# Kernel optimization log

Hardware: AMD Instinct MI355X
Metric: run time of the kernel (lower is better)

## Reference

```python
import jax, jax.numpy as jnp
import numpy as np

B, D, HW, Z, PATCH = 16, 768, 32, 256, 16
N = HW * HW          # input_token_num = 1024
TOPK = N // 2        # topk=0.5 -> 512
EPS = 1e-5

def setup_inputs() -> dict:
    key = jax.random.key(0)
    ks = jax.random.split(key, 9)
    s = 0.02
    return {
        'image_features': jax.random.normal(ks[0], (B, D, HW, HW), jnp.float32),
        'w1': jax.random.normal(ks[1], (D, D), jnp.float32) * s,
        'b1': jnp.zeros((D,), jnp.float32),
        'w2': jax.random.normal(ks[2], (D, 1), jnp.float32) * s,
        'b2': jnp.zeros((1,), jnp.float32),
        'wp': jax.random.normal(ks[3], (D, Z), jnp.float32) * s,   # pre_projection
        'bp': jnp.zeros((Z,), jnp.float32),
        'mask_token': jnp.zeros((Z, 1), jnp.float32),              # init mode 0
        'conv_w': jax.random.normal(ks[4], (Z, Z), jnp.float32) * s,  # post_projection 1x1
        'conv_b': jnp.zeros((Z,), jnp.float32),
    }

def _upsample_nearest(m, f):
    # (B,1,h,w) -> (B,1,h*f,w*f)
    return jnp.repeat(jnp.repeat(m, f, axis=2), f, axis=3)

def reference(image_features, w1, b1, w2, b2, wp, bp, mask_token, conv_w, conv_b):
    x = image_features.transpose(0, 2, 3, 1).reshape(B, N, D)  # B (H W) C
    # score MLP: Linear-ReLU-Linear-Sigmoid
    h = jax.nn.relu(jnp.einsum('bnd,de->bne', x, w1) + b1)
    pred_score = jax.nn.sigmoid(jnp.einsum('bnd,de->bne', h, w2) + b2).reshape(B, N)
    score_sg = jax.lax.stop_gradient(pred_score)  # clone().detach()
    order = jnp.argsort(-score_sg, axis=1)        # descending sort
    top = order[:, :TOPK]                          # (B, K) int
    # LayerNorm (no affine) over channel dim
    mu = x.mean(-1, keepdims=True)
    var = x.var(-1, keepdims=True)
    xn = (x - mu) * jax.lax.rsqrt(var + EPS)
    # gather topk tokens, weight by (non-detached) score
    gathered = jnp.take_along_axis(xn, top[..., None], axis=1)
    gathered = gathered * jnp.take_along_axis(pred_score, top, axis=1)[..., None]
    sample_h = (jnp.einsum('bkd,dz->bkz', gathered, wp) + bp).transpose(0, 2, 1)  # B Z K
    # binary mask: scatter ones at topk positions
    mask = jnp.zeros((B, N), jnp.float32).at[jnp.arange(B)[:, None], top].set(1.0)
    binary_map = _upsample_nearest(mask.reshape(B, 1, HW, HW), PATCH)
    # normalized score map (global min/max over whole batch)
    smin, smax = score_sg.min(), score_sg.max()
    normed = (score_sg - smin) / jnp.maximum(smax - smin, EPS)
    score_map = _upsample_nearest(normed.reshape(B, 1, HW, HW), PATCH)
    # postforward: fill all N slots with mask_token, scatter sample_h at topk slots
    base = jnp.broadcast_to(mask_token, (Z, N))
    emb = jax.vmap(lambda hi, idx: base.at[:, idx].set(hi))(sample_h, top)  # (B,Z,N)
    emb = emb.reshape(B, Z, HW, HW)
    dec = jnp.einsum('oz,bzhw->bohw', conv_w, emb) + conv_b[None, :, None, None]
    return dec, binary_map, score_map
```

## Files before the change

### kernel.cpp

```cpp
#include <hip/hip_runtime.h>
#include <hip/hip_bf16.h>
#include <math.h>

#define B_ 16
#define D_ 768
#define N_ 1024
#define Z_ 256
#define TOPK_ 512
#define HW_ 32
#define EPS_ 1e-5f

typedef unsigned int uint;
typedef unsigned short ushort;
typedef __attribute__((ext_vector_type(4))) short short4v;
typedef __attribute__((ext_vector_type(8))) short bf16x8;
typedef __attribute__((ext_vector_type(4))) float f32x4;
typedef __attribute__((ext_vector_type(4))) int int4v;

__device__ __forceinline__ ushort f2bf(float v) {
  uint b = __float_as_uint(v);
  b += 0x7FFFu + ((b >> 16) & 1u);
  return (ushort)(b >> 16);
}
__device__ __forceinline__ float bf2f(ushort h) { return __uint_as_float(((uint)h) << 16); }
__device__ __forceinline__ int pk2(ushort a, ushort b) { return (int)((uint)a | ((uint)b << 16)); }

__global__ __launch_bounds__(256) void k_pre1(const float* __restrict__ conv_w,
                                              const float* __restrict__ conv_b,
                                              const float* __restrict__ bp,
                                              const float* __restrict__ mtk,
                                              float* __restrict__ db,
                                              float* __restrict__ bg) {
  int o = threadIdx.x;
  float a1 = 0.f, a2 = 0.f;
  for (int z = 0; z < Z_; ++z) {
    float c = conv_w[o * Z_ + z];
    a1 += c * bp[z];
    a2 += c * mtk[z];
  }
  db[o] = conv_b[o] + a1;
  bg[o] = conv_b[o] + a2;
}

__global__ __launch_bounds__(64) void k_w1pack(const float* __restrict__ w1,
                                               short* __restrict__ wA) {
  int lane = threadIdx.x;
  int f = blockIdx.x;
  int eg = f / 24, kkg = f % 24;
  int e = eg * 16 + (lane & 15);
  int d0 = kkg * 32 + 8 * (lane >> 4);
  ushort hh[8], ll[8];
#pragma unroll
  for (int j = 0; j < 8; ++j) {
    float v = w1[(size_t)(d0 + j) * D_ + e];
    hh[j] = f2bf(v);
    ll[j] = f2bf(v - bf2f(hh[j]));
  }
  int4v ph = {pk2(hh[0],hh[1]), pk2(hh[2],hh[3]), pk2(hh[4],hh[5]), pk2(hh[6],hh[7])};
  int4v pl = {pk2(ll[0],ll[1]), pk2(ll[2],ll[3]), pk2(ll[4],ll[5]), pk2(ll[6],ll[7])};
  int4v* W = (int4v*)wA;
  W[(size_t)f * 128 + lane] = ph;
  W[(size_t)f * 128 + 64 + lane] = pl;
}

__global__ __launch_bounds__(64) void k_mtpack(const float* __restrict__ wp,
                                               const float* __restrict__ conv_w,
                                               short* __restrict__ mtA) {
  int lane = threadIdx.x;
  int f = blockIdx.x;
  int og = f / 24, kkg = f % 24;
  int o = og * 16 + (lane & 15);
  int d0 = kkg * 32 + 8 * (lane >> 4);
  float acc[8] = {0.f,0.f,0.f,0.f,0.f,0.f,0.f,0.f};
  for (int z = 0; z < Z_; ++z) {
    float c = conv_w[o * Z_ + z];
#pragma unroll
    for (int j = 0; j < 8; ++j) acc[j] += wp[(size_t)(d0 + j) * Z_ + z] * c;
  }
  int4v p = {pk2(f2bf(acc[0]),f2bf(acc[1])), pk2(f2bf(acc[2]),f2bf(acc[3])),
             pk2(f2bf(acc[4]),f2bf(acc[5])), pk2(f2bf(acc[6]),f2bf(acc[7]))};
  ((int4v*)mtA)[(size_t)f * 64 + lane] = p;
}

__global__ __launch_bounds__(512, 2) void k_score_mfma(const float* __restrict__ xin,
                                                       const short* __restrict__ wA,
                                                       const float* __restrict__ b1,
                                                       const float* __restrict__ w2,
                                                       const float* __restrict__ b2,
                                                       float* __restrict__ score) {
  __shared__ short panH[64 * 128];
  __shared__ short panL[64 * 128];
  __shared__ float red[8][4][16];
  int tid = threadIdx.x;
  int wave = tid >> 6, lane = tid & 63;
  int g = lane >> 4, cc = lane & 15;
  int b = blockIdx.x >> 4;
  int n0 = (blockIdx.x & 15) * 64;
  const float* xb = xin + (size_t)b * D_ * N_ + n0;
  int qt = tid & 15, qd = tid >> 4;
  int t0 = qt * 4, dl0 = qd * 4;
  f32x4 acc[6][4];
#pragma unroll
  for (int et = 0; et < 6; ++et)
#pragma unroll
    for (int tn = 0; tn < 4; ++tn) acc[et][tn] = (f32x4){0.f,0.f,0.f,0.f};
  const int4v* Ab = (const int4v*)wA;
  for (int kc = 0; kc < 6; ++kc) {
    float4 v0 = *(const float4*)(xb + (size_t)(kc*128 + dl0 + 0) * N_ + t0);
    float4 v1 = *(const float4*)(xb + (size_t)(kc*128 + dl0 + 1) * N_ + t0);
    float4 v2 = *(const float4*)(xb + (size_t)(kc*128 + dl0 + 2) * N_ + t0);
    float4 v3 = *(const float4*)(xb + (size_t)(kc*128 + dl0 + 3) * N_ + t0);
    __syncthreads();
#define STG(j, e0, e1, e2, e3) { \
    int t = t0 + (j); \
    int sb = t * 128 + (dl0 ^ ((t & 7) << 3)); \
    ushort h0 = f2bf(e0), h1 = f2bf(e1), h2 = f2bf(e2), h3 = f2bf(e3); \
    short4v ph = {(short)h0,(short)h1,(short)h2,(short)h3}; \
    short4v pl = {(short)f2bf((e0)-bf2f(h0)), (short)f2bf((e1)-bf2f(h1)), \
                  (short)f2bf((e2)-bf2f(h2)), (short)f2bf((e3)-bf2f(h3))}; \
    *(short4v*)&panH[sb] = ph; \
    *(short4v*)&panL[sb] = pl; }
    STG(0, v0.x, v1.x, v2.x, v3.x)
    STG(1, v0.y, v1.y, v2.y, v3.y)
    STG(2, v0.z, v1.z, v2.z, v3.z)
    STG(3, v0.w, v1.w, v2.w, v3.w)
#undef STG
    __syncthreads();
#pragma unroll
    for (int kk = 0; kk < 4; ++kk) {
      bf16x8 Bh[4], Bl[4];
#pragma unroll
      for (int tn = 0; tn < 4; ++tn) {
        int t = tn * 16 + cc;
        int sb = t * 128 + ((kk * 32 + 8 * g) ^ ((t & 7) << 3));
        Bh[tn] = *(const bf16x8*)&panH[sb];
        Bl[tn] = *(const bf16x8*)&panL[sb];
      }
#pragma unroll
      for (int et = 0; et < 6; ++et) {
        size_t fidx = ((size_t)((wave * 6 + et) * 24 + (kc * 4 + kk))) * 128 + lane;
        union { int4v i; bf16x8 v; } ah, al;
        ah.i = Ab[fidx];
        al.i = Ab[fidx + 64];
#pragma unroll
        for (int tn = 0; tn < 4; ++tn) {
          acc[et][tn] = __builtin_amdgcn_mfma_f32_16x16x32_bf16(ah.v, Bh[tn], acc[et][tn], 0, 0, 0);
          acc[et][tn] = __builtin_amdgcn_mfma_f32_16x16x32_bf16(ah.v, Bl[tn], acc[et][tn], 0, 0, 0);
          acc[et][tn] = __builtin_amdgcn_mfma_f32_16x16x32_bf16(al.v, Bh[tn], acc[et][tn], 0, 0, 0);
        }
      }
    }
  }
  float lg[4] = {0.f,0.f,0.f,0.f};
#pragma unroll
  for (int et = 0; et < 6; ++et) {
    int e = wave * 96 + et * 16 + 4 * g;
    float4 bb = *(const float4*)(b1 + e);
    float4 ww = *(const float4*)(w2 + e);
#pragma unroll
    for (int tn = 0; tn < 4; ++tn) {
      lg[tn] += fmaxf(acc[et][tn][0] + bb.x, 0.f) * ww.x;
      lg[tn] += fmaxf(acc[et][tn][1] + bb.y, 0.f) * ww.y;
      lg[tn] += fmaxf(acc[et][tn][2] + bb.z, 0.f) * ww.z;
      lg[tn] += fmaxf(acc[et][tn][3] + bb.w, 0.f) * ww.w;
    }
  }
#pragma unroll
  for (int tn = 0; tn < 4; ++tn) {
    lg[tn] += __shfl_xor(lg[tn], 16, 64);
    lg[tn] += __shfl_xor(lg[tn], 32, 64);
  }
  if (lane < 16) {
#pragma unroll
    for (int tn = 0; tn < 4; ++tn) red[wave][tn][lane] = lg[tn];
  }
  __syncthreads();
  if (tid < 64) {
    float v = b2[0];
#pragma unroll
    for (int w = 0; w < 8; ++w) v += red[w][tid >> 4][tid & 15];
    score[b * N_ + n0 + tid] = 1.f / (1.f + expf(-v));
  }
}

__global__ __launch_bounds__(1024) void k_select(const float* __restrict__ score,
                                                 int* __restrict__ rank,
                                                 float* __restrict__ mm) {
  __shared__ float s[N_];
  __shared__ float red[32];
  int tid = threadIdx.x;
  int b = blockIdx.x >> 2;
  int tg = blockIdx.x & 3;
  s[tid] = score[b * N_ + tid];
  __syncthreads();
  int token = tg * 256 + (tid >> 2);
  int jq = tid & 3;
  float si = s[token];
  int cnt = 0;
  int j0 = jq * 256;
  for (int j = j0; j < j0 + 256; j += 4) {
    float4 sj = *reinterpret_cast<const float4*>(&s[j]);
    cnt += (sj.x > si) || (sj.x == si && (j + 0) < token);
    cnt += (sj.y > si) || (sj.y == si && (j + 1) < token);
    cnt += (sj.z > si) || (sj.z == si && (j + 2) < token);
    cnt += (sj.w > si) || (sj.w == si && (j + 3) < token);
  }
  cnt += __shfl_xor(cnt, 1, 64);
  cnt += __shfl_xor(cnt, 2, 64);
  if (jq == 0) rank[b * N_ + token] = cnt;
  if (tg == 0) {
    float v = s[tid];
    float mn = v, mx = v;
#pragma unroll
    for (int off = 32; off > 0; off >>= 1) {
      mn = fminf(mn, __shfl_xor(mn, off, 64));
      mx = fmaxf(mx, __shfl_xor(mx, off, 64));
    }
    if ((tid & 63) == 0) { red[tid >> 6] = mn; red[16 + (tid >> 6)] = mx; }
    __syncthreads();
    if (tid == 0) {
      float a = red[0], c = red[16];
      for (int w = 1; w < 16; ++w) { a = fminf(a, red[w]); c = fmaxf(c, red[16 + w]); }
      mm[2 * b] = a; mm[2 * b + 1] = c;
    }
  }
}

__global__ __launch_bounds__(512) void k_gather_t(const float* __restrict__ xin,
                                                  const float* __restrict__ score,
                                                  const int* __restrict__ rank,
                                                  short* __restrict__ gtT) {
  __shared__ float pan[32][769];
  __shared__ float sw1[8][32], sw2[8][32];
  __shared__ float ssc[32], ssh[32];
  __shared__ int rkv[32];
  int tid = threadIdx.x;
  int b = blockIdx.x >> 5;
  int n0 = (blockIdx.x & 31) * 32;
  int qt = tid & 7, dbs = tid >> 3;
  const float* xb = xin + (size_t)b * D_ * N_ + n0 + qt * 4;
  float a0=0.f,a1=0.f,a2=0.f,a3=0.f,q0=0.f,q1=0.f,q2=0.f,q3=0.f;
#pragma unroll
  for (int it = 0; it < 12; ++it) {
    int d = it * 64 + dbs;
    float4 v = *(const float4*)(xb + (size_t)d * N_);
    pan[qt*4+0][d] = v.x; pan[qt*4+1][d] = v.y; pan[qt*4+2][d] = v.z; pan[qt*4+3][d] = v.w;
    a0 += v.x; q0 += v.x*v.x; a1 += v.y; q1 += v.y*v.y;
    a2 += v.z; q2 += v.z*v.z; a3 += v.w; q3 += v.w*v.w;
  }
#pragma unroll
  for (int m = 8; m <= 32; m <<= 1) {
    a0 += __shfl_xor(a0, m, 64); q0 += __shfl_xor(q0, m, 64);
    a1 += __shfl_xor(a1, m, 64); q1 += __shfl_xor(q1, m, 64);
    a2 += __shfl_xor(a2, m, 64); q2 += __shfl_xor(q2, m, 64);
    a3 += __shfl_xor(a3, m, 64); q3 += __shfl_xor(q3, m, 64);
  }
  int lane = tid & 63, wave = tid >> 6;
  if (lane < 8) {
    sw1[wave][lane*4+0] = a0; sw2[wave][lane*4+0] = q0;
    sw1[wave][lane*4+1] = a1; sw2[wave][lane*4+1] = q1;
    sw1[wave][lane*4+2] = a2; sw2[wave][lane*4+2] = q2;
    sw1[wave][lane*4+3] = a3; sw2[wave][lane*4+3] = q3;
  }
  __syncthreads();
  if (tid < 32) {
    float S = 0.f, Q = 0.f;
#pragma unroll
    for (int w = 0; w < 8; ++w) { S += sw1[w][tid]; Q += sw2[w][tid]; }
    float mu = S * (1.f / D_);
    float var = Q * (1.f / D_) - mu * mu;
    float rs = rsqrtf(var + EPS_);
    float sc = rs * score[b * N_ + n0 + tid];
    ssc[tid] = sc; ssh[tid] = -mu * sc;
    rkv[tid] = rank[b * N_ + n0 + tid];
  }
  __syncthreads();
  for (int t = 0; t < 32; ++t) {
    int rk = rkv[t];
    if (rk < TOPK_ && tid < 384) {
      float sc = ssc[t], sh = ssh[t];
      float u0 = pan[t][2*tid]   * sc + sh;
      float u1 = pan[t][2*tid+1] * sc + sh;
      ((uint*)(gtT + ((size_t)(b * TOPK_ + rk)) * D_))[tid] =
          (uint)f2bf(u0) | ((uint)f2bf(u1) << 16);
    }
  }
}

__global__ __launch_bounds__(512, 2) void k_gemm2m(const short* __restrict__ gtT,
                                                   const short* __restrict__ mtA,
                                                   const float* __restrict__ db,
                                                   float* __restrict__ dselT) {
  __shared__ short pan[64 * 128];
  int tid = threadIdx.x;
  int wave = tid >> 6, lane = tid & 63;
  int g = lane >> 4, cc = lane & 15;
  int b = blockIdx.x >> 3, kt = blockIdx.x & 7;
  int srow = tid >> 3, scol = (tid & 7) * 16;
  const short* gb = gtT + (size_t)(b * TOPK_ + kt * 64) * D_;
  f32x4 acc[2][4];
#pragma unroll
  for (int et = 0; et < 2; ++et)
#pragma unroll
    for (int tn = 0; tn < 4; ++tn) acc[et][tn] = (f32x4){0.f,0.f,0.f,0.f};
  const int4v* Am = (const int4v*)mtA;
  for (int kc = 0; kc < 6; ++kc) {
    int4v u0 = *(const int4v*)(gb + (size_t)srow * D_ + kc*128 + scol);
    int4v u1 = *(const int4v*)(gb + (size_t)srow * D_ + kc*128 + scol + 8);
    __syncthreads();
    int sz = (srow & 7) << 3;
    *(int4v*)&pan[srow * 128 + (scol ^ sz)] = u0;
    *(int4v*)&pan[srow * 128 + ((scol + 8) ^ sz)] = u1;
    __syncthreads();
#pragma unroll
    for (int kk = 0; kk < 4; ++kk) {
      bf16x8 Bv[4];
#pragma unroll
      for (int tn = 0; tn < 4; ++tn) {
        int t = tn * 16 + cc;
        int sb = t * 128 + ((kk * 32 + 8 * g) ^ ((t & 7) << 3));
        Bv[tn] = *(const bf16x8*)&pan[sb];
      }
#pragma unroll
      for (int et = 0; et < 2; ++et) {
        size_t fidx = ((size_t)((wave * 2 + et) * 24 + (kc * 4 + kk))) * 64 + lane;
        union { int4v i; bf16x8 v; } av; av.i = Am[fidx];
#pragma unroll
        for (int tn = 0; tn < 4; ++tn)
          acc[et][tn] = __builtin_amdgcn_mfma_f32_16x16x32_bf16(av.v, Bv[tn], acc[et][tn], 0, 0, 0);
      }
    }
  }
#pragma unroll
  for (int et = 0; et < 2; ++et) {
    int o0 = wave * 32 + et * 16 + 4 * g;
#pragma unroll
    for (int r = 0; r < 4; ++r) {
      int o = o0 + r;
      float dbv = db[o];
      float* orow = dselT + ((size_t)(b * Z_ + o)) * TOPK_ + kt * 64 + cc;
      orow[0]  = acc[et][0][r] + dbv;
      orow[16] = acc[et][1][r] + dbv;
      orow[32] = acc[et][2][r] + dbv;
      orow[48] = acc[et][3][r] + dbv;
    }
  }
}

__global__ __launch_bounds__(256) void k_dec(const float* __restrict__ dselT,
                                             const float* __restrict__ bg,
                                             const int* __restrict__ rank,
                                             float* __restrict__ out) {
  __shared__ float row[TOPK_];
  __shared__ int rks[N_];
  int tid = threadIdx.x;
  int b = blockIdx.x >> 8;
  int o = blockIdx.x & 255;
  row[tid]       = dselT[((size_t)(b * Z_ + o)) * TOPK_ + tid];
  row[tid + 256] = dselT[((size_t)(b * Z_ + o)) * TOPK_ + tid + 256];
#pragma unroll
  for (int r = 0; r < 4; ++r) rks[r*256+tid] = rank[b * N_ + r*256 + tid];
  __syncthreads();
  float bgv = bg[o];
  float* orow = out + ((size_t)(b * Z_ + o)) * N_;
#pragma unroll
  for (int r = 0; r < 4; ++r) {
    int rk = rks[r*256+tid];
    orow[r*256+tid] = (rk < TOPK_) ? row[rk] : bgv;
  }
}

__global__ __launch_bounds__(128) void k_maps(const float* __restrict__ score,
                                              const int* __restrict__ rank,
                                              const float* __restrict__ mm,
                                              float* __restrict__ out) {
  int tid = threadIdx.x;
  int b = blockIdx.x >> 9;
  int ph = blockIdx.x & 511;
  float mn = mm[0], mx = mm[1];
#pragma unroll
  for (int w = 1; w < 16; ++w) { mn = fminf(mn, mm[2 * w]); mx = fmaxf(mx, mm[2 * w + 1]); }
  float inv = 1.f / fmaxf(mx - mn, EPS_);
  int pw0 = tid * 4;
  int cell = (ph >> 4) * HW_ + (pw0 >> 4);
  int rk = rank[b * N_ + cell];
  float bin = (rk < TOPK_) ? 1.f : 0.f;
  float sv = (score[b * N_ + cell] - mn) * inv;
  size_t base = (size_t)b * (512 * 512) + (size_t)ph * 512 + pw0;
  float4 bv = {bin, bin, bin, bin};
  float4 svv = {sv, sv, sv, sv};
  *reinterpret_cast<float4*>(out + 4194304 + base) = bv;
  *reinterpret_cast<float4*>(out + 8388608 + base) = svv;
}

extern "C" void kernel_launch(void* const* d_in, const int* in_sizes, int n_in,
                              void* d_out, int out_size, void* d_ws, size_t ws_size,
                              hipStream_t stream) {
  const float* xin = (const float*)d_in[0];
  const float* w1  = (const float*)d_in[1];
  const float* b1  = (const float*)d_in[2];
  const float* w2  = (const float*)d_in[3];
  const float* b2  = (const float*)d_in[4];
  const float* wp  = (const float*)d_in[5];
  const float* bp  = (const float*)d_in[6];
  const float* mtk = (const float*)d_in[7];
  const float* cw  = (const float*)d_in[8];
  const float* cb  = (const float*)d_in[9];
  float* out = (float*)d_out;

  short* wA   = (short*)d_ws;
  short* mtA  = wA + 1179648;
  short* gtT  = mtA + 196608;
  float* db   = (float*)(gtT + 6291456);
  float* bg   = db + 256;
  float* score = bg + 256;
  float* mm   = score + 16384;
  int*   rank = (int*)(mm + 32);
  float* dselT = (float*)(rank + 16384);

  k_pre1      <<<dim3(1),    dim3(256),  0, stream>>>(cw, cb, bp, mtk, db, bg);
  k_w1pack    <<<dim3(1152), dim3(64),   0, stream>>>(w1, wA);
  k_mtpack    <<<dim3(384),  dim3(64),   0, stream>>>(wp, cw, mtA);
  k_score_mfma<<<dim3(256),  dim3(512),  0, stream>>>(xin, wA, b1, w2, b2, score);
  k_select    <<<dim3(64),   dim3(1024), 0, stream>>>(score, rank, mm);
  k_gather_t  <<<dim3(512),  dim3(512),  0, stream>>>(xin, score, rank, gtT);
  k_gemm2m    <<<dim3(128),  dim3(512),  0, stream>>>(gtT, mtA, db, dselT);
  k_dec       <<<dim3(4096), dim3(256),  0, stream>>>(dselT, bg, rank, out);
  k_maps      <<<dim3(8192), dim3(128),  0, stream>>>(score, rank, mm, out);
}
```

Measured before the change: 253.9 us.

## Split score and projection GEMMs across more blocks; hoist LayerNorm stats into a separate kernel

The score GEMM now splits the hidden dimension across two blocks per token tile and combines partial logits with atomics into a zeroed buffer. The sigmoid moves into the selection kernel. LayerNorm statistics get their own kernel so the gather kernel can split channels into halves. The second GEMM uses smaller tiles and more blocks. Weight-prep kernels (bias fold, conv weight transpose, merged-weight pack) are parallelised, and the LDS swizzle gains an extra XOR term. The goal is better occupancy and CU coverage on the mid-sized kernels, at the cost of extra launches, an extra pass over the input for statistics, and atomics.

```diff
diff --git a/kernel.cpp b/kernel.cpp
--- a/kernel.cpp
+++ b/kernel.cpp
@@ -25,21 +25,46 @@
 __device__ __forceinline__ float bf2f(ushort h) { return __uint_as_float(((uint)h) << 16); }
 __device__ __forceinline__ int pk2(ushort a, ushort b) { return (int)((uint)a | ((uint)b << 16)); }
 
-__global__ __launch_bounds__(256) void k_pre1(const float* __restrict__ conv_w,
-                                              const float* __restrict__ conv_b,
-                                              const float* __restrict__ bp,
-                                              const float* __restrict__ mtk,
-                                              float* __restrict__ db,
-                                              float* __restrict__ bg) {
-  int o = threadIdx.x;
-  float a1 = 0.f, a2 = 0.f;
-  for (int z = 0; z < Z_; ++z) {
-    float c = conv_w[o * Z_ + z];
-    a1 += c * bp[z];
-    a2 += c * mtk[z];
-  }
-  db[o] = conv_b[o] + a1;
-  bg[o] = conv_b[o] + a2;
+__global__ __launch_bounds__(1024) void k_zero(float* __restrict__ logit) {
+  logit[blockIdx.x * 1024 + threadIdx.x] = 0.f;
+}
+
+__global__ __launch_bounds__(256) void k_db(const float* __restrict__ cw,
+                                            const float* __restrict__ cb,
+                                            const float* __restrict__ bp,
+                                            const float* __restrict__ mtk,
+                                            float* __restrict__ db,
+                                            float* __restrict__ bg) {
+  __shared__ float s1[4], s2[4];
+  int o = blockIdx.x, tid = threadIdx.x;
+  float c = cw[o * Z_ + tid];
+  float a1 = c * bp[tid], a2 = c * mtk[tid];
+#pragma unroll
+  for (int m = 32; m > 0; m >>= 1) { a1 += __shfl_xor(a1, m, 64); a2 += __shfl_xor(a2, m, 64); }
+  if ((tid & 63) == 0) { s1[tid >> 6] = a1; s2[tid >> 6] = a2; }
+  __syncthreads();
+  if (tid == 0) {
+    db[o] = cb[o] + s1[0] + s1[1] + s1[2] + s1[3];
+    bg[o] = cb[o] + s2[0] + s2[1] + s2[2] + s2[3];
+  }
+}
+
+__global__ __launch_bounds__(256) void k_cwT(const float* __restrict__ cw,
+                                             float* __restrict__ cwT) {
+  __shared__ float tile[32][33];
+  int bx = blockIdx.x & 7, by = blockIdx.x >> 3;
+  int tid = threadIdx.x;
+#pragma unroll
+  for (int it = 0; it < 4; ++it) {
+    int idx = it * 256 + tid, r = idx >> 5, c = idx & 31;
+    tile[r][c] = cw[(size_t)(by * 32 + r) * Z_ + bx * 32 + c];
+  }
+  __syncthreads();
+#pragma unroll
+  for (int it = 0; it < 4; ++it) {
+    int idx = it * 256 + tid, r = idx >> 5, c = idx & 31;
+    cwT[(size_t)(bx * 32 + r) * Z_ + by * 32 + c] = tile[c][r];
+  }
 }
 
 __global__ __launch_bounds__(64) void k_w1pack(const float* __restrict__ w1,
@@ -63,48 +88,73 @@
   W[(size_t)f * 128 + 64 + lane] = pl;
 }
 
-__global__ __launch_bounds__(64) void k_mtpack(const float* __restrict__ wp,
-                                               const float* __restrict__ conv_w,
-                                               short* __restrict__ mtA) {
-  int lane = threadIdx.x;
-  int f = blockIdx.x;
-  int og = f / 24, kkg = f % 24;
-  int o = og * 16 + (lane & 15);
-  int d0 = kkg * 32 + 8 * (lane >> 4);
+__global__ __launch_bounds__(256) void k_mtpA(const float* __restrict__ wp,
+                                              const float* __restrict__ cwT,
+                                              short* __restrict__ mtA) {
+  int o = threadIdx.x;
+  int d0 = blockIdx.x * 8;
+  int kkg = blockIdx.x >> 2, g = blockIdx.x & 3;
   float acc[8] = {0.f,0.f,0.f,0.f,0.f,0.f,0.f,0.f};
   for (int z = 0; z < Z_; ++z) {
-    float c = conv_w[o * Z_ + z];
+    float c = cwT[(size_t)z * Z_ + o];
 #pragma unroll
     for (int j = 0; j < 8; ++j) acc[j] += wp[(size_t)(d0 + j) * Z_ + z] * c;
   }
+  int og = o >> 4, lane = (o & 15) + 16 * g;
   int4v p = {pk2(f2bf(acc[0]),f2bf(acc[1])), pk2(f2bf(acc[2]),f2bf(acc[3])),
              pk2(f2bf(acc[4]),f2bf(acc[5])), pk2(f2bf(acc[6]),f2bf(acc[7]))};
-  ((int4v*)mtA)[(size_t)f * 64 + lane] = p;
-}
-
-__global__ __launch_bounds__(512, 2) void k_score_mfma(const float* __restrict__ xin,
+  ((int4v*)mtA)[(size_t)(og * 24 + kkg) * 64 + lane] = p;
+}
+
+__global__ __launch_bounds__(256) void k_stats(const float* __restrict__ xin,
+                                               float* __restrict__ rs_out,
+                                               float* __restrict__ mu_out) {
+  __shared__ float rs[4][64], rs2[4][64];
+  int tid = threadIdx.x;
+  int b = blockIdx.x >> 4;
+  int n = (blockIdx.x & 15) * 64 + (tid & 63);
+  int p = tid >> 6;
+  float s = 0.f, s2 = 0.f;
+  for (int d = p; d < D_; d += 4) {
+    float v = xin[((size_t)b * D_ + d) * N_ + n];
+    s += v; s2 += v * v;
+  }
+  rs[p][tid & 63] = s; rs2[p][tid & 63] = s2;
+  __syncthreads();
+  if (p == 0) {
+    float S = rs[0][tid] + rs[1][tid] + rs[2][tid] + rs[3][tid];
+    float S2 = rs2[0][tid] + rs2[1][tid] + rs2[2][tid] + rs2[3][tid];
+    float m = S * (1.f / D_);
+    float var = S2 * (1.f / D_) - m * m;
+    mu_out[b * N_ + n] = m;
+    rs_out[b * N_ + n] = rsqrtf(var + EPS_);
+  }
+}
+
+__global__ __launch_bounds__(512, 4) void k_score_mfma(const float* __restrict__ xin,
                                                        const short* __restrict__ wA,
                                                        const float* __restrict__ b1,
                                                        const float* __restrict__ w2,
-                                                       const float* __restrict__ b2,
-                                                       float* __restrict__ score) {
+                                                       float* __restrict__ logit) {
   __shared__ short panH[64 * 128];
   __shared__ short panL[64 * 128];
   __shared__ float red[8][4][16];
   int tid = threadIdx.x;
   int wave = tid >> 6, lane = tid & 63;
   int g = lane >> 4, cc = lane & 15;
-  int b = blockIdx.x >> 4;
-  int n0 = (blockIdx.x & 15) * 64;
+  int tile = blockIdx.x & 255, eh = blockIdx.x >> 8;
+  int b = tile >> 4;
+  int n0 = (tile & 15) * 64;
   const float* xb = xin + (size_t)b * D_ * N_ + n0;
   int qt = tid & 15, qd = tid >> 4;
   int t0 = qt * 4, dl0 = qd * 4;
-  f32x4 acc[6][4];
-#pragma unroll
-  for (int et = 0; et < 6; ++et)
+  f32x4 acc[3][4];
+#pragma unroll
+  for (int et = 0; et < 3; ++et)
 #pragma unroll
     for (int tn = 0; tn < 4; ++tn) acc[et][tn] = (f32x4){0.f,0.f,0.f,0.f};
   const int4v* Ab = (const int4v*)wA;
+  int eg0 = eh * 24 + wave * 3;
   for (int kc = 0; kc < 6; ++kc) {
     float4 v0 = *(const float4*)(xb + (size_t)(kc*128 + dl0 + 0) * N_ + t0);
     float4 v1 = *(const float4*)(xb + (size_t)(kc*128 + dl0 + 1) * N_ + t0);
@@ -113,7 +163,8 @@
     __syncthreads();
 #define STG(j, e0, e1, e2, e3) { \
     int t = t0 + (j); \
-    int sb = t * 128 + (dl0 ^ ((t & 7) << 3)); \
+    int g1 = ((t & 7) ^ (t >> 3)); \
+    int sb = t * 128 + (dl0 ^ (g1 << 3)); \
     ushort h0 = f2bf(e0), h1 = f2bf(e1), h2 = f2bf(e2), h3 = f2bf(e3); \
     short4v ph = {(short)h0,(short)h1,(short)h2,(short)h3}; \
     short4v pl = {(short)f2bf((e0)-bf2f(h0)), (short)f2bf((e1)-bf2f(h1)), \
@@ -132,13 +183,14 @@
 #pragma unroll
       for (int tn = 0; tn < 4; ++tn) {
         int t = tn * 16 + cc;
-        int sb = t * 128 + ((kk * 32 + 8 * g) ^ ((t & 7) << 3));
+        int g1 = ((t & 7) ^ (t >> 3));
+        int sb = t * 128 + ((kk * 32 + 8 * g) ^ (g1 << 3));
         Bh[tn] = *(const bf16x8*)&panH[sb];
         Bl[tn] = *(const bf16x8*)&panL[sb];
       }
 #pragma unroll
-      for (int et = 0; et < 6; ++et) {
-        size_t fidx = ((size_t)((wave * 6 + et) * 24 + (kc * 4 + kk))) * 128 + lane;
+      for (int et = 0; et < 3; ++et) {
+        size_t fidx = ((size_t)((eg0 + et) * 24 + (kc * 4 + kk))) * 128 + lane;
         union { int4v i; bf16x8 v; } ah, al;
         ah.i = Ab[fidx];
         al.i = Ab[fidx + 64];
@@ -153,8 +205,8 @@
   }
   float lg[4] = {0.f,0.f,0.f,0.f};
 #pragma unroll
-  for (int et = 0; et < 6; ++et) {
-    int e = wave * 96 + et * 16 + 4 * g;
+  for (int et = 0; et < 3; ++et) {
+    int e = (eg0 + et) * 16 + 4 * g;
     float4 bb = *(const float4*)(b1 + e);
     float4 ww = *(const float4*)(w2 + e);
 #pragma unroll
@@ -176,14 +228,16 @@
   }
   __syncthreads();
   if (tid < 64) {
-    float v = b2[0];
+    float v = 0.f;
 #pragma unroll
     for (int w = 0; w < 8; ++w) v += red[w][tid >> 4][tid & 15];
-    score[b * N_ + n0 + tid] = 1.f / (1.f + expf(-v));
-  }
-}
-
-__global__ __launch_bounds__(1024) void k_select(const float* __restrict__ score,
+    atomicAdd(&logit[b * N_ + n0 + tid], v);
+  }
+}
+
+__global__ __launch_bounds__(1024) void k_select(const float* __restrict__ logit,
+                                                 const float* __restrict__ b2,
+                                                 float* __restrict__ score,
                                                  int* __restrict__ rank,
                                                  float* __restrict__ mm) {
   __shared__ float s[N_];
@@ -191,7 +245,9 @@
   int tid = threadIdx.x;
   int b = blockIdx.x >> 2;
   int tg = blockIdx.x & 3;
-  s[tid] = score[b * N_ + tid];
+  float b2v = b2[0];
+  float sv0 = 1.f / (1.f + expf(-(logit[b * N_ + tid] + b2v)));
+  s[tid] = sv0;
   __syncthreads();
   int token = tg * 256 + (tid >> 2);
   int jq = tid & 3;
@@ -209,8 +265,8 @@
   cnt += __shfl_xor(cnt, 2, 64);
   if (jq == 0) rank[b * N_ + token] = cnt;
   if (tg == 0) {
-    float v = s[tid];
-    float mn = v, mx = v;
+    score[b * N_ + tid] = sv0;
+    float mn = sv0, mx = sv0;
 #pragma unroll
     for (int off = 32; off > 0; off >>= 1) {
       mn = fminf(mn, __shfl_xor(mn, off, 64));
@@ -226,123 +282,105 @@
   }
 }
 
-__global__ __launch_bounds__(512) void k_gather_t(const float* __restrict__ xin,
-                                                  const float* __restrict__ score,
-                                                  const int* __restrict__ rank,
-                                                  short* __restrict__ gtT) {
-  __shared__ float pan[32][769];
-  __shared__ float sw1[8][32], sw2[8][32];
+__global__ __launch_bounds__(256) void k_gath(const float* __restrict__ xin,
+                                              const float* __restrict__ score,
+                                              const float* __restrict__ rs,
+                                              const float* __restrict__ mu,
+                                              const int* __restrict__ rank,
+                                              short* __restrict__ gtT) {
+  __shared__ float pan[32][389];
   __shared__ float ssc[32], ssh[32];
   __shared__ int rkv[32];
   int tid = threadIdx.x;
-  int b = blockIdx.x >> 5;
-  int n0 = (blockIdx.x & 31) * 32;
-  int qt = tid & 7, dbs = tid >> 3;
-  const float* xb = xin + (size_t)b * D_ * N_ + n0 + qt * 4;
-  float a0=0.f,a1=0.f,a2=0.f,a3=0.f,q0=0.f,q1=0.f,q2=0.f,q3=0.f;
+  int bid = blockIdx.x;
+  int b = bid >> 6;
+  int nt = (bid & 63) >> 1, dh = bid & 1;
+  int n0 = nt * 32, d0 = dh * 384;
+  int qt = tid & 7, qd = tid >> 3;
+  const float* xb = xin + ((size_t)b * D_ + d0) * N_ + n0 + qt * 4;
 #pragma unroll
   for (int it = 0; it < 12; ++it) {
-    int d = it * 64 + dbs;
+    int d = it * 32 + qd;
     float4 v = *(const float4*)(xb + (size_t)d * N_);
     pan[qt*4+0][d] = v.x; pan[qt*4+1][d] = v.y; pan[qt*4+2][d] = v.z; pan[qt*4+3][d] = v.w;
-    a0 += v.x; q0 += v.x*v.x; a1 += v.y; q1 += v.y*v.y;
-    a2 += v.z; q2 += v.z*v.z; a3 += v.w; q3 += v.w*v.w;
-  }
-#pragma unroll
-  for (int m = 8; m <= 32; m <<= 1) {
-    a0 += __shfl_xor(a0, m, 64); q0 += __shfl_xor(q0, m, 64);
-    a1 += __shfl_xor(a1, m, 64); q1 += __shfl_xor(q1, m, 64);
-    a2 += __shfl_xor(a2, m, 64); q2 += __shfl_xor(q2, m, 64);
-    a3 += __shfl_xor(a3, m, 64); q3 += __shfl_xor(q3, m, 64);
-  }
-  int lane = tid & 63, wave = tid >> 6;
-  if (lane < 8) {
-    sw1[wave][lane*4+0] = a0; sw2[wave][lane*4+0] = q0;
-    sw1[wave][lane*4+1] = a1; sw2[wave][lane*4+1] = q1;
-    sw1[wave][lane*4+2] = a2; sw2[wave][lane*4+2] = q2;
-    sw1[wave][lane*4+3] = a3; sw2[wave][lane*4+3] = q3;
-  }
-  __syncthreads();
+  }
   if (tid < 32) {
-    float S = 0.f, Q = 0.f;
-#pragma unroll
-    for (int w = 0; w < 8; ++w) { S += sw1[w][tid]; Q += sw2[w][tid]; }
-    float mu = S * (1.f / D_);
-    float var = Q * (1.f / D_) - mu * mu;
-    float rs = rsqrtf(var + EPS_);
-    float sc = rs * score[b * N_ + n0 + tid];
-    ssc[tid] = sc; ssh[tid] = -mu * sc;
-    rkv[tid] = rank[b * N_ + n0 + tid];
+    int n = b * N_ + n0 + tid;
+    float sc = rs[n] * score[n];
+    ssc[tid] = sc; ssh[tid] = -mu[n] * sc;
+    rkv[tid] = rank[n];
   }
   __syncthreads();
   for (int t = 0; t < 32; ++t) {
     int rk = rkv[t];
-    if (rk < TOPK_ && tid < 384) {
+    if (rk < TOPK_ && tid < 192) {
       float sc = ssc[t], sh = ssh[t];
       float u0 = pan[t][2*tid]   * sc + sh;
       float u1 = pan[t][2*tid+1] * sc + sh;
-      ((uint*)(gtT + ((size_t)(b * TOPK_ + rk)) * D_))[tid] =
+      ((uint*)(gtT + ((size_t)(b * TOPK_ + rk)) * D_ + d0))[tid] =
           (uint)f2bf(u0) | ((uint)f2bf(u1) << 16);
     }
   }
 }
 
-__global__ __launch_bounds__(512, 2) void k_gemm2m(const short* __restrict__ gtT,
+__global__ __launch_bounds__(256, 4) void k_gemm2m(const short* __restrict__ gtT,
                                                    const short* __restrict__ mtA,
                                                    const float* __restrict__ db,
                                                    float* __restrict__ dselT) {
-  __shared__ short pan[64 * 128];
+  __shared__ short pan[32 * 128];
   int tid = threadIdx.x;
   int wave = tid >> 6, lane = tid & 63;
   int g = lane >> 4, cc = lane & 15;
-  int b = blockIdx.x >> 3, kt = blockIdx.x & 7;
+  int bid = blockIdx.x;
+  int b = bid >> 5, kt = (bid & 31) >> 1, oh = bid & 1;
   int srow = tid >> 3, scol = (tid & 7) * 16;
-  const short* gb = gtT + (size_t)(b * TOPK_ + kt * 64) * D_;
-  f32x4 acc[2][4];
+  const short* gb = gtT + (size_t)(b * TOPK_ + kt * 32) * D_;
+  f32x4 acc[2][2];
 #pragma unroll
   for (int et = 0; et < 2; ++et)
 #pragma unroll
-    for (int tn = 0; tn < 4; ++tn) acc[et][tn] = (f32x4){0.f,0.f,0.f,0.f};
+    for (int tn = 0; tn < 2; ++tn) acc[et][tn] = (f32x4){0.f,0.f,0.f,0.f};
   const int4v* Am = (const int4v*)mtA;
+  int sg1 = ((srow & 7) ^ (srow >> 3)) << 3;
   for (int kc = 0; kc < 6; ++kc) {
     int4v u0 = *(const int4v*)(gb + (size_t)srow * D_ + kc*128 + scol);
     int4v u1 = *(const int4v*)(gb + (size_t)srow * D_ + kc*128 + scol + 8);
     __syncthreads();
-    int sz = (srow & 7) << 3;
-    *(int4v*)&pan[srow * 128 + (scol ^ sz)] = u0;
-    *(int4v*)&pan[srow * 128 + ((scol + 8) ^ sz)] = u1;
+    *(int4v*)&pan[srow * 128 + (scol ^ sg1)] = u0;
+    *(int4v*)&pan[srow * 128 + ((scol + 8) ^ sg1)] = u1;
     __syncthreads();
 #pragma unroll
     for (int kk = 0; kk < 4; ++kk) {
-      bf16x8 Bv[4];
-#pragma unroll
-      for (int tn = 0; tn < 4; ++tn) {
+      bf16x8 Bv[2];
+#pragma unroll
+      for (int tn = 0; tn < 2; ++tn) {
         int t = tn * 16 + cc;
-        int sb = t * 128 + ((kk * 32 + 8 * g) ^ ((t & 7) << 3));
+        int g1 = ((t & 7) ^ (t >> 3));
+        int sb = t * 128 + ((kk * 32 + 8 * g) ^ (g1 << 3));
         Bv[tn] = *(const bf16x8*)&pan[sb];
       }
 #pragma unroll
       for (int et = 0; et < 2; ++et) {
-        size_t fidx = ((size_t)((wave * 2 + et) * 24 + (kc * 4 + kk))) * 64 + lane;
+        int og = oh * 8 + wave * 2 + et;
+        size_t fidx = ((size_t)(og * 24 + (kc * 4 + kk))) * 64 + lane;
         union { int4v i; bf16x8 v; } av; av.i = Am[fidx];
 #pragma unroll
-        for (int tn = 0; tn < 4; ++tn)
+        for (int tn = 0; tn < 2; ++tn)
           acc[et][tn] = __builtin_amdgcn_mfma_f32_16x16x32_bf16(av.v, Bv[tn], acc[et][tn], 0, 0, 0);
       }
     }
   }
 #pragma unroll
   for (int et = 0; et < 2; ++et) {
-    int o0 = wave * 32 + et * 16 + 4 * g;
+    int og = oh * 8 + wave * 2 + et;
+    int o0 = og * 16 + 4 * g;
 #pragma unroll
     for (int r = 0; r < 4; ++r) {
       int o = o0 + r;
       float dbv = db[o];
-      float* orow = dselT + ((size_t)(b * Z_ + o)) * TOPK_ + kt * 64 + cc;
+      float* orow = dselT + ((size_t)(b * Z_ + o)) * TOPK_ + kt * 32 + cc;
       orow[0]  = acc[et][0][r] + dbv;
       orow[16] = acc[et][1][r] + dbv;
-      orow[32] = acc[et][2][r] + dbv;
-      orow[48] = acc[et][3][r] + dbv;
     }
   }
 }
@@ -408,23 +446,30 @@
   const float* cb  = (const float*)d_in[9];
   float* out = (float*)d_out;
 
-  short* wA   = (short*)d_ws;
-  short* mtA  = wA + 1179648;
-  short* gtT  = mtA + 196608;
-  float* db   = (float*)(gtT + 6291456);
-  float* bg   = db + 256;
-  float* score = bg + 256;
-  float* mm   = score + 16384;
-  int*   rank = (int*)(mm + 32);
+  short* wA    = (short*)d_ws;
+  short* mtA   = wA + 1179648;
+  short* gtT   = mtA + 196608;
+  float* cwT   = (float*)(gtT + 6291456);
+  float* db    = cwT + 65536;
+  float* bg    = db + 256;
+  float* logit = bg + 256;
+  float* score = logit + 16384;
+  float* rs    = score + 16384;
+  float* mu    = rs + 16384;
+  float* mm    = mu + 16384;
+  int*   rank  = (int*)(mm + 32);
   float* dselT = (float*)(rank + 16384);
 
-  k_pre1      <<<dim3(1),    dim3(256),  0, stream>>>(cw, cb, bp, mtk, db, bg);
+  k_zero      <<<dim3(16),   dim3(1024), 0, stream>>>(logit);
+  k_db        <<<dim3(256),  dim3(256),  0, stream>>>(cw, cb, bp, mtk, db, bg);
+  k_cwT       <<<dim3(64),   dim3(256),  0, stream>>>(cw, cwT);
   k_w1pack    <<<dim3(1152), dim3(64),   0, stream>>>(w1, wA);
-  k_mtpack    <<<dim3(384),  dim3(64),   0, stream>>>(wp, cw, mtA);
-  k_score_mfma<<<dim3(256),  dim3(512),  0, stream>>>(xin, wA, b1, w2, b2, score);
-  k_select    <<<dim3(64),   dim3(1024), 0, stream>>>(score, rank, mm);
-  k_gather_t  <<<dim3(512),  dim3(512),  0, stream>>>(xin, score, rank, gtT);
-  k_gemm2m    <<<dim3(128),  dim3(512),  0, stream>>>(gtT, mtA, db, dselT);
+  k_mtpA      <<<dim3(96),   dim3(256),  0, stream>>>(wp, cwT, mtA);
+  k_stats     <<<dim3(256),  dim3(256),  0, stream>>>(xin, rs, mu);
+  k_score_mfma<<<dim3(512),  dim3(512),  0, stream>>>(xin, wA, b1, w2, logit);
+  k_select    <<<dim3(64),   dim3(1024), 0, stream>>>(logit, b2, score, rank, mm);
+  k_gath      <<<dim3(1024), dim3(256),  0, stream>>>(xin, score, rs, mu, rank, gtT);
+  k_gemm2m    <<<dim3(512),  dim3(256),  0, stream>>>(gtT, mtA, db, dselT);
   k_dec       <<<dim3(4096), dim3(256),  0, stream>>>(dselT, bg, rank, out);
   k_maps      <<<dim3(8192), dim3(128),  0, stream>>>(score, rank, mm, out);
 }
```

Result: slower. 306.2 us (+20.6%).
